# Optimization experiments

Hardware: AMD Instinct MI355X
Metric: run time of the kernel (lower is better)

The kernel has to match this reference:

```python
import jax, jax.numpy as jnp
import numpy as np

B, N, D = 32, 1024, 256

def setup_inputs() -> dict:
    key = jax.random.key(0)
    ks = jax.random.split(key, 7)
    s = 1.0 / np.sqrt(D)
    return {
        "traj": jax.random.normal(ks[0], (B, N, D), dtype=jnp.float32),
        "Wq": jax.random.normal(ks[1], (D, D), dtype=jnp.float32) * s,
        "bq": jax.random.normal(ks[2], (D,), dtype=jnp.float32) * s,
        "Wk": jax.random.normal(ks[3], (D, D), dtype=jnp.float32) * s,
        "bk": jax.random.normal(ks[4], (D,), dtype=jnp.float32) * s,
        "Wv": jax.random.normal(ks[5], (D, D), dtype=jnp.float32) * s,
        "bv": jax.random.normal(ks[6], (D,), dtype=jnp.float32) * s,
    }

def reference(traj, Wq, bq, Wk, bk, Wv, bv):
    # torch nn.Linear: y = x @ W.T + b
    q = jnp.einsum('bnd,ed->bne', traj, Wq) + bq  # [B,N,D]
    k = jnp.einsum('bnd,ed->bne', traj, Wk) + bk  # [B,N,D]
    v = jnp.einsum('bnd,ed->bne', traj, Wv) + bv  # [B,N,D]
    # unscaled dot-product attention (original sums broadcasted Q*K over D)
    scores = jnp.einsum('bnd,bmd->bnm', q, k)     # [B,N,N]
    attn = jax.nn.softmax(scores, axis=-1)        # [B,N,N]
    out = jnp.einsum('bnm,bmd->bnd', attn, v)     # [B,N,D]
    return out
```

## Files before the change

kernel.cpp:

```cpp
#include <hip/hip_runtime.h>

#define NN 1024
#define DD 256

typedef __attribute__((ext_vector_type(8))) _Float16 f16x8;
typedef __attribute__((ext_vector_type(4))) float f32x4;

union H8 { f16x8 v; _Float16 s[8]; };

__device__ __forceinline__ void g2lds16(const void* g, void* l) {
  __builtin_amdgcn_global_load_lds(
      (const __attribute__((address_space(1))) void*)g,
      (__attribute__((address_space(3))) void*)l, 16, 0, 0);
}

__global__ void wconv_kernel(const float* __restrict__ Wq, const float* __restrict__ Wk,
                             const float* __restrict__ Wv, _Float16* __restrict__ pw) {
  int c = blockIdx.x * 256 + threadIdx.x;
  int lane = c & 63;
  int nt = (c >> 6) & 1;
  int kk = (c >> 7) & 7;
  int et = c >> 10;
  int e = et * 32 + nt * 16 + (lane & 15);
  int d = kk * 32 + (lane >> 4) * 8;
  const float* W = (e < 256) ? Wq : (e < 512 ? Wk : Wv);
  const float* src = W + (e & 255) * 256 + d;
  H8 xx;
  for (int j = 0; j < 8; ++j) xx.s[j] = (_Float16)src[j];
  *(f16x8*)(pw + (size_t)c * 8) = xx.v;
}

__global__ __launch_bounds__(256, 2) void proj_kernel(
    const float* __restrict__ traj,
    const float* __restrict__ bq, const float* __restrict__ bk, const float* __restrict__ bv,
    const _Float16* __restrict__ pw,
    _Float16* __restrict__ pq, _Float16* __restrict__ pk, _Float16* __restrict__ pv)
{
  __shared__ alignas(16) _Float16 Wl[2][8192];
  __shared__ alignas(16) _Float16 Cs[4][1280];

  const int t = threadIdx.x;
  const int lane = t & 63, wave = t >> 6;
  const int col16 = lane & 15, quad = lane >> 4;
  const int mt = blockIdx.x >> 1, eh = blockIdx.x & 1;
  const int mbase = mt * 128;
  const int bb = mbase >> 10;

  f16x8 aq[2][8];
  for (int s = 0; s < 2; ++s) {
    const float* ap = traj + (size_t)(mbase + wave * 32 + s * 16 + col16) * DD;
    for (int kk = 0; kk < 8; ++kk) {
      float4 u0 = *(const float4*)(ap + kk * 32 + quad * 8);
      float4 u1 = *(const float4*)(ap + kk * 32 + quad * 8 + 4);
      H8 xx;
      xx.s[0] = (_Float16)u0.x; xx.s[1] = (_Float16)u0.y;
      xx.s[2] = (_Float16)u0.z; xx.s[3] = (_Float16)u0.w;
      xx.s[4] = (_Float16)u1.x; xx.s[5] = (_Float16)u1.y;
      xx.s[6] = (_Float16)u1.z; xx.s[7] = (_Float16)u1.w;
      aq[s][kk] = xx.v;
    }
  }

  const f32x4 zero = {0.f, 0.f, 0.f, 0.f};
  const int et0 = eh * 12;

  for (int i = 0; i < 4; ++i)
    g2lds16(pw + (size_t)et0 * 8192 + (size_t)(i * 256 + t) * 8, Wl[0] + (i * 256 + t) * 8);

  for (int ei = 0; ei < 12; ++ei) {
    __syncthreads();
    if (ei < 11) {
      const _Float16* ws = pw + (size_t)(et0 + ei + 1) * 8192;
      _Float16* wd = Wl[(ei + 1) & 1];
      for (int i = 0; i < 4; ++i)
        g2lds16(ws + (size_t)(i * 256 + t) * 8, wd + (i * 256 + t) * 8);
    }
    const _Float16* wl = Wl[ei & 1];

    f32x4 acc[2][2];
    acc[0][0] = zero; acc[0][1] = zero; acc[1][0] = zero; acc[1][1] = zero;
    for (int kk = 0; kk < 8; ++kk)
      for (int nt = 0; nt < 2; ++nt) {
        f16x8 bw = *(const f16x8*)&wl[((kk * 2 + nt) * 64 + lane) * 8];
        acc[0][nt] = __builtin_amdgcn_mfma_f32_16x16x32_f16(aq[0][kk], bw, acc[0][nt], 0, 0, 0);
        acc[1][nt] = __builtin_amdgcn_mfma_f32_16x16x32_f16(aq[1][kk], bw, acc[1][nt], 0, 0, 0);
      }

    int e0 = eh * 384 + ei * 32;
    int sel = e0 >> 8;
    const float* bias = (sel == 0) ? bq : (sel == 1 ? bk : bv);
    for (int nt = 0; nt < 2; ++nt) {
      float bvl = bias[(e0 & 255) + nt * 16 + col16];
      for (int s = 0; s < 2; ++s) {
        acc[s][nt][0] += bvl; acc[s][nt][1] += bvl;
        acc[s][nt][2] += bvl; acc[s][nt][3] += bvl;
      }
    }

    _Float16* cs = Cs[wave];
    if (sel < 2) {
      for (int s = 0; s < 2; ++s)
        for (int nt = 0; nt < 2; ++nt)
          for (int r = 0; r < 4; ++r)
            cs[(s * 16 + quad * 4 + r) * 40 + nt * 16 + col16] = (_Float16)acc[s][nt][r];
      if (sel == 0) {
        for (int s = 0; s < 2; ++s) {
          f16x8 val = *(const f16x8*)&cs[(s * 16 + col16) * 40 + quad * 8];
          int g = (mbase >> 4) + wave * 2 + s;
          *(f16x8*)(pq + (size_t)((g * 8 + ei) * 64 + lane) * 8) = val;
        }
      } else {
        int kkg = (e0 - 256) >> 5;
        for (int s = 0; s < 2; ++s) {
          f16x8 val = *(const f16x8*)&cs[(s * 16 + col16) * 40 + quad * 8];
          int kgg = ((mbase & 1023) >> 4) + wave * 2 + s;
          *(f16x8*)(pk + (size_t)(((bb * 64 + kgg) * 8 + kkg) * 64 + lane) * 8) = val;
        }
      }
    } else {
      for (int s = 0; s < 2; ++s)
        for (int nt = 0; nt < 2; ++nt)
          for (int r = 0; r < 4; ++r)
            cs[(nt * 16 + col16) * 40 + s * 16 + quad * 4 + r] = (_Float16)acc[s][nt][r];
      int kt32 = ((mbase & 1023) >> 5) + wave;
      for (int dtl = 0; dtl < 2; ++dtl) {
        f16x8 val = *(const f16x8*)&cs[(dtl * 16 + col16) * 40 + quad * 8];
        int dtg = ((e0 - 512) >> 4) + dtl;
        *(f16x8*)(pv + (size_t)(((bb * 32 + kt32) * 16 + dtg) * 64 + lane) * 8) = val;
      }
    }
  }
}

__global__ __launch_bounds__(256, 3) void attn_kernel(
    const _Float16* __restrict__ pq, const _Float16* __restrict__ pk,
    const _Float16* __restrict__ pv, float* __restrict__ out)
{
  __shared__ alignas(16) _Float16 Ks[2][8192];
  __shared__ alignas(16) _Float16 Vs[8192];

  const int t = threadIdx.x;
  const int lane = t & 63, wave = t >> 6;
  const int col16 = lane & 15, quad = lane >> 4;
  const int b = blockIdx.x, qt = blockIdx.y;
  const int qrow0 = b * NN + qt * 64;

  f16x8 aq[8];
  {
    int g = b * 64 + qt * 4 + wave;
    for (int kk = 0; kk < 8; ++kk)
      aq[kk] = *(const f16x8*)(pq + (size_t)((g * 8 + kk) * 64 + lane) * 8);
  }

  float m_i = -3.0e38f, l_i = 0.f;
  f32x4 O[16];
  const f32x4 zero = {0.f, 0.f, 0.f, 0.f};
  for (int dt = 0; dt < 16; ++dt) O[dt] = zero;

  const _Float16* kbb = pk + (size_t)b * 64 * 8 * 64 * 8;
  const _Float16* vbb = pv + (size_t)b * 32 * 16 * 64 * 8;

  for (int i = 0; i < 4; ++i)
    g2lds16(kbb + (size_t)(i * 256 + t) * 8, Ks[0] + (i * 256 + t) * 8);

  for (int kt = 0; kt < 32; ++kt) {
    __syncthreads();
    {
      const _Float16* vg = vbb + (size_t)kt * 8192;
      for (int i = 0; i < 4; ++i)
        g2lds16(vg + (size_t)(i * 256 + t) * 8, Vs + (i * 256 + t) * 8);
      if (kt < 31) {
        const _Float16* kg = kbb + (size_t)(kt + 1) * 8192;
        _Float16* kd = Ks[(kt + 1) & 1];
        for (int i = 0; i < 4; ++i)
          g2lds16(kg + (size_t)(i * 256 + t) * 8, kd + (i * 256 + t) * 8);
      }
    }

    const _Float16* ks = Ks[kt & 1];
    f32x4 S[2]; S[0] = zero; S[1] = zero;
    for (int kk = 0; kk < 8; ++kk)
      for (int nt = 0; nt < 2; ++nt) {
        f16x8 bk_ = *(const f16x8*)&ks[((nt * 8 + kk) * 64 + lane) * 8];
        S[nt] = __builtin_amdgcn_mfma_f32_16x16x32_f16(aq[kk], bk_, S[nt], 0, 0, 0);
      }

    __syncthreads();

    float* Sp = (float*)Ks[kt & 1];
    for (int nt = 0; nt < 2; ++nt)
      for (int r = 0; r < 4; ++r)
        Sp[(wave * 16 + quad * 4 + r) * 36 + nt * 16 + col16] = S[nt][r];
    float sv[8];
    *(f32x4*)&sv[0] = *(const f32x4*)&Sp[(wave * 16 + col16) * 36 + quad * 8];
    *(f32x4*)&sv[4] = *(const f32x4*)&Sp[(wave * 16 + col16) * 36 + quad * 8 + 4];

    float vmax = sv[0];
    for (int j = 1; j < 8; ++j) vmax = fmaxf(vmax, sv[j]);
    vmax = fmaxf(vmax, __shfl_xor(vmax, 16));
    vmax = fmaxf(vmax, __shfl_xor(vmax, 32));
    float nm = fmaxf(m_i, vmax);
    float alpha = __expf(m_i - nm);
    float rs = 0.f;
    H8 px;
    for (int j = 0; j < 8; ++j) {
      float pj = __expf(sv[j] - nm);
      rs += pj;
      px.s[j] = (_Float16)pj;
    }
    rs += __shfl_xor(rs, 16);
    rs += __shfl_xor(rs, 32);
    l_i = l_i * alpha + rs;
    m_i = nm;
    f16x8 ap = px.v;

    if (__ballot(alpha < 1.0f)) {
      float a4[4];
      for (int r = 0; r < 4; ++r) a4[r] = __shfl(alpha, quad * 4 + r);
      for (int dt = 0; dt < 16; ++dt)
        for (int r = 0; r < 4; ++r) O[dt][r] *= a4[r];
    }

    for (int dt = 0; dt < 16; ++dt) {
      f16x8 bv_ = *(const f16x8*)&Vs[(dt * 64 + lane) * 8];
      O[dt] = __builtin_amdgcn_mfma_f32_16x16x32_f16(ap, bv_, O[dt], 0, 0, 0);
    }
  }

  float linv[4];
  for (int r = 0; r < 4; ++r) linv[r] = 1.0f / __shfl(l_i, quad * 4 + r);
  for (int r = 0; r < 4; ++r) {
    float* orow = out + (size_t)(qrow0 + wave * 16 + quad * 4 + r) * DD;
    for (int dt = 0; dt < 16; ++dt)
      orow[dt * 16 + col16] = O[dt][r] * linv[r];
  }
}

extern "C" void kernel_launch(void* const* d_in, const int* in_sizes, int n_in,
                              void* d_out, int out_size, void* d_ws, size_t ws_size,
                              hipStream_t stream) {
  const float* traj = (const float*)d_in[0];
  const float* Wq   = (const float*)d_in[1];
  const float* bq   = (const float*)d_in[2];
  const float* Wk   = (const float*)d_in[3];
  const float* bk   = (const float*)d_in[4];
  const float* Wv   = (const float*)d_in[5];
  const float* bv   = (const float*)d_in[6];

  _Float16* pq = (_Float16*)d_ws;
  _Float16* pk = pq + (size_t)32768 * 256;
  _Float16* pv = pk + (size_t)32768 * 256;
  _Float16* pw = pv + (size_t)32768 * 256;

  wconv_kernel<<<96, 256, 0, stream>>>(Wq, Wk, Wv, pw);
  proj_kernel<<<512, 256, 0, stream>>>(traj, bq, bk, bv, pw, pq, pk, pv);
  attn_kernel<<<dim3(32, 16), 256, 0, stream>>>(pq, pk, pv, (float*)d_out);
}
```

Measured before the change: 170.3 us.

## Double query rows per attention block, double-buffer V, prepack traj, restructure projection

The attention kernel now processes 128 query rows per block (two 16-row tiles per wave), so each K/V tile loaded into LDS is reused twice as much. V gets double-buffered alongside K, and scores go through a dedicated per-wave LDS scratch, which removes one block barrier per iteration. A separate kernel prepacks traj into fp16 MFMA layout. The projection kernel is split four ways over output columns and loads its whole weight slice into LDS up front. The cost is half as many attention blocks (256 on a large GPU), more registers per wave, an extra pass over traj, and a larger grid for the projection.

```diff
diff --git a/kernel.cpp b/kernel.cpp
--- a/kernel.cpp
+++ b/kernel.cpp
@@ -12,6 +12,17 @@
   __builtin_amdgcn_global_load_lds(
       (const __attribute__((address_space(1))) void*)g,
       (__attribute__((address_space(3))) void*)l, 16, 0, 0);
+}
+
+__global__ void apack_kernel(const float* __restrict__ traj, _Float16* __restrict__ pa) {
+  int c = blockIdx.x * 256 + threadIdx.x;
+  int lane = c & 63;
+  int kk = (c >> 6) & 7;
+  int g = c >> 9;
+  const float* src = traj + (size_t)(g * 16 + (lane & 15)) * 256 + kk * 32 + (lane >> 4) * 8;
+  H8 xx;
+  for (int j = 0; j < 8; ++j) xx.s[j] = (_Float16)src[j];
+  *(f16x8*)(pa + (size_t)c * 8) = xx.v;
 }
 
 __global__ void wconv_kernel(const float* __restrict__ Wq, const float* __restrict__ Wk,
@@ -30,63 +41,49 @@
   *(f16x8*)(pw + (size_t)c * 8) = xx.v;
 }
 
-__global__ __launch_bounds__(256, 2) void proj_kernel(
-    const float* __restrict__ traj,
+__global__ __launch_bounds__(256, 1) void proj_kernel(
+    const _Float16* __restrict__ pa,
     const float* __restrict__ bq, const float* __restrict__ bk, const float* __restrict__ bv,
     const _Float16* __restrict__ pw,
     _Float16* __restrict__ pq, _Float16* __restrict__ pk, _Float16* __restrict__ pv)
 {
-  __shared__ alignas(16) _Float16 Wl[2][8192];
+  __shared__ alignas(16) _Float16 Wl[49152];
   __shared__ alignas(16) _Float16 Cs[4][1280];
 
   const int t = threadIdx.x;
   const int lane = t & 63, wave = t >> 6;
   const int col16 = lane & 15, quad = lane >> 4;
-  const int mt = blockIdx.x >> 1, eh = blockIdx.x & 1;
+  const int mt = blockIdx.x >> 2, eq = blockIdx.x & 3;
   const int mbase = mt * 128;
   const int bb = mbase >> 10;
 
+  {
+    const _Float16* ws = pw + (size_t)eq * 6 * 8192;
+    for (int i = 0; i < 24; ++i)
+      g2lds16(ws + (size_t)(i * 256 + t) * 8, Wl + (i * 256 + t) * 8);
+  }
+
   f16x8 aq[2][8];
   for (int s = 0; s < 2; ++s) {
-    const float* ap = traj + (size_t)(mbase + wave * 32 + s * 16 + col16) * DD;
-    for (int kk = 0; kk < 8; ++kk) {
-      float4 u0 = *(const float4*)(ap + kk * 32 + quad * 8);
-      float4 u1 = *(const float4*)(ap + kk * 32 + quad * 8 + 4);
-      H8 xx;
-      xx.s[0] = (_Float16)u0.x; xx.s[1] = (_Float16)u0.y;
-      xx.s[2] = (_Float16)u0.z; xx.s[3] = (_Float16)u0.w;
-      xx.s[4] = (_Float16)u1.x; xx.s[5] = (_Float16)u1.y;
-      xx.s[6] = (_Float16)u1.z; xx.s[7] = (_Float16)u1.w;
-      aq[s][kk] = xx.v;
-    }
-  }
-
+    int g = (mbase >> 4) + wave * 2 + s;
+    for (int kk = 0; kk < 8; ++kk)
+      aq[s][kk] = *(const f16x8*)(pa + (size_t)((g * 8 + kk) * 64 + lane) * 8);
+  }
+
+  __syncthreads();
   const f32x4 zero = {0.f, 0.f, 0.f, 0.f};
-  const int et0 = eh * 12;
-
-  for (int i = 0; i < 4; ++i)
-    g2lds16(pw + (size_t)et0 * 8192 + (size_t)(i * 256 + t) * 8, Wl[0] + (i * 256 + t) * 8);
-
-  for (int ei = 0; ei < 12; ++ei) {
-    __syncthreads();
-    if (ei < 11) {
-      const _Float16* ws = pw + (size_t)(et0 + ei + 1) * 8192;
-      _Float16* wd = Wl[(ei + 1) & 1];
-      for (int i = 0; i < 4; ++i)
-        g2lds16(ws + (size_t)(i * 256 + t) * 8, wd + (i * 256 + t) * 8);
-    }
-    const _Float16* wl = Wl[ei & 1];
-
+
+  for (int ei = 0; ei < 6; ++ei) {
     f32x4 acc[2][2];
     acc[0][0] = zero; acc[0][1] = zero; acc[1][0] = zero; acc[1][1] = zero;
     for (int kk = 0; kk < 8; ++kk)
       for (int nt = 0; nt < 2; ++nt) {
-        f16x8 bw = *(const f16x8*)&wl[((kk * 2 + nt) * 64 + lane) * 8];
+        f16x8 bw = *(const f16x8*)&Wl[((ei * 16 + kk * 2 + nt) * 64 + lane) * 8];
         acc[0][nt] = __builtin_amdgcn_mfma_f32_16x16x32_f16(aq[0][kk], bw, acc[0][nt], 0, 0, 0);
         acc[1][nt] = __builtin_amdgcn_mfma_f32_16x16x32_f16(aq[1][kk], bw, acc[1][nt], 0, 0, 0);
       }
 
-    int e0 = eh * 384 + ei * 32;
+    int e0 = eq * 192 + ei * 32;
     int sel = e0 >> 8;
     const float* bias = (sel == 0) ? bq : (sel == 1 ? bk : bv);
     for (int nt = 0; nt < 2; ++nt) {
@@ -104,10 +101,11 @@
           for (int r = 0; r < 4; ++r)
             cs[(s * 16 + quad * 4 + r) * 40 + nt * 16 + col16] = (_Float16)acc[s][nt][r];
       if (sel == 0) {
+        int kkq = e0 >> 5;
         for (int s = 0; s < 2; ++s) {
           f16x8 val = *(const f16x8*)&cs[(s * 16 + col16) * 40 + quad * 8];
           int g = (mbase >> 4) + wave * 2 + s;
-          *(f16x8*)(pq + (size_t)((g * 8 + ei) * 64 + lane) * 8) = val;
+          *(f16x8*)(pq + (size_t)((g * 8 + kkq) * 64 + lane) * 8) = val;
         }
       } else {
         int kkg = (e0 - 256) >> 5;
@@ -132,107 +130,123 @@
   }
 }
 
-__global__ __launch_bounds__(256, 3) void attn_kernel(
+__global__ __launch_bounds__(256, 1) void attn_kernel(
     const _Float16* __restrict__ pq, const _Float16* __restrict__ pk,
     const _Float16* __restrict__ pv, float* __restrict__ out)
 {
   __shared__ alignas(16) _Float16 Ks[2][8192];
-  __shared__ alignas(16) _Float16 Vs[8192];
+  __shared__ alignas(16) _Float16 Vs[2][8192];
+  __shared__ alignas(16) float Sp[4][1056];
 
   const int t = threadIdx.x;
   const int lane = t & 63, wave = t >> 6;
   const int col16 = lane & 15, quad = lane >> 4;
   const int b = blockIdx.x, qt = blockIdx.y;
-  const int qrow0 = b * NN + qt * 64;
-
-  f16x8 aq[8];
-  {
-    int g = b * 64 + qt * 4 + wave;
+  const int qrow0 = b * NN + qt * 128;
+
+  f16x8 aq[2][8];
+  for (int s = 0; s < 2; ++s) {
+    int g = b * 64 + qt * 8 + wave * 2 + s;
     for (int kk = 0; kk < 8; ++kk)
-      aq[kk] = *(const f16x8*)(pq + (size_t)((g * 8 + kk) * 64 + lane) * 8);
-  }
-
-  float m_i = -3.0e38f, l_i = 0.f;
-  f32x4 O[16];
+      aq[s][kk] = *(const f16x8*)(pq + (size_t)((g * 8 + kk) * 64 + lane) * 8);
+  }
+
+  float m_i[2] = {-3.0e38f, -3.0e38f}, l_i[2] = {0.f, 0.f};
+  f32x4 O[2][16];
   const f32x4 zero = {0.f, 0.f, 0.f, 0.f};
-  for (int dt = 0; dt < 16; ++dt) O[dt] = zero;
+  for (int s = 0; s < 2; ++s)
+    for (int dt = 0; dt < 16; ++dt) O[s][dt] = zero;
 
   const _Float16* kbb = pk + (size_t)b * 64 * 8 * 64 * 8;
   const _Float16* vbb = pv + (size_t)b * 32 * 16 * 64 * 8;
 
   for (int i = 0; i < 4; ++i)
     g2lds16(kbb + (size_t)(i * 256 + t) * 8, Ks[0] + (i * 256 + t) * 8);
+  for (int i = 0; i < 4; ++i)
+    g2lds16(vbb + (size_t)(i * 256 + t) * 8, Vs[0] + (i * 256 + t) * 8);
 
   for (int kt = 0; kt < 32; ++kt) {
     __syncthreads();
-    {
-      const _Float16* vg = vbb + (size_t)kt * 8192;
+    if (kt < 31) {
+      const _Float16* kg = kbb + (size_t)(kt + 1) * 8192;
+      const _Float16* vg = vbb + (size_t)(kt + 1) * 8192;
+      _Float16* kd = Ks[(kt + 1) & 1];
+      _Float16* vd = Vs[(kt + 1) & 1];
       for (int i = 0; i < 4; ++i)
-        g2lds16(vg + (size_t)(i * 256 + t) * 8, Vs + (i * 256 + t) * 8);
-      if (kt < 31) {
-        const _Float16* kg = kbb + (size_t)(kt + 1) * 8192;
-        _Float16* kd = Ks[(kt + 1) & 1];
-        for (int i = 0; i < 4; ++i)
-          g2lds16(kg + (size_t)(i * 256 + t) * 8, kd + (i * 256 + t) * 8);
-      }
+        g2lds16(kg + (size_t)(i * 256 + t) * 8, kd + (i * 256 + t) * 8);
+      for (int i = 0; i < 4; ++i)
+        g2lds16(vg + (size_t)(i * 256 + t) * 8, vd + (i * 256 + t) * 8);
     }
 
     const _Float16* ks = Ks[kt & 1];
-    f32x4 S[2]; S[0] = zero; S[1] = zero;
-    for (int kk = 0; kk < 8; ++kk)
-      for (int nt = 0; nt < 2; ++nt) {
-        f16x8 bk_ = *(const f16x8*)&ks[((nt * 8 + kk) * 64 + lane) * 8];
-        S[nt] = __builtin_amdgcn_mfma_f32_16x16x32_f16(aq[kk], bk_, S[nt], 0, 0, 0);
-      }
-
-    __syncthreads();
-
-    float* Sp = (float*)Ks[kt & 1];
-    for (int nt = 0; nt < 2; ++nt)
-      for (int r = 0; r < 4; ++r)
-        Sp[(wave * 16 + quad * 4 + r) * 36 + nt * 16 + col16] = S[nt][r];
-    float sv[8];
-    *(f32x4*)&sv[0] = *(const f32x4*)&Sp[(wave * 16 + col16) * 36 + quad * 8];
-    *(f32x4*)&sv[4] = *(const f32x4*)&Sp[(wave * 16 + col16) * 36 + quad * 8 + 4];
-
-    float vmax = sv[0];
-    for (int j = 1; j < 8; ++j) vmax = fmaxf(vmax, sv[j]);
-    vmax = fmaxf(vmax, __shfl_xor(vmax, 16));
-    vmax = fmaxf(vmax, __shfl_xor(vmax, 32));
-    float nm = fmaxf(m_i, vmax);
-    float alpha = __expf(m_i - nm);
-    float rs = 0.f;
-    H8 px;
-    for (int j = 0; j < 8; ++j) {
-      float pj = __expf(sv[j] - nm);
-      rs += pj;
-      px.s[j] = (_Float16)pj;
-    }
-    rs += __shfl_xor(rs, 16);
-    rs += __shfl_xor(rs, 32);
-    l_i = l_i * alpha + rs;
-    m_i = nm;
-    f16x8 ap = px.v;
-
-    if (__ballot(alpha < 1.0f)) {
-      float a4[4];
-      for (int r = 0; r < 4; ++r) a4[r] = __shfl(alpha, quad * 4 + r);
+    f32x4 S[2][2];
+    S[0][0] = zero; S[0][1] = zero; S[1][0] = zero; S[1][1] = zero;
+    for (int kk = 0; kk < 8; ++kk) {
+      f16x8 bk0 = *(const f16x8*)&ks[((0 * 8 + kk) * 64 + lane) * 8];
+      f16x8 bk1 = *(const f16x8*)&ks[((1 * 8 + kk) * 64 + lane) * 8];
+      S[0][0] = __builtin_amdgcn_mfma_f32_16x16x32_f16(aq[0][kk], bk0, S[0][0], 0, 0, 0);
+      S[0][1] = __builtin_amdgcn_mfma_f32_16x16x32_f16(aq[0][kk], bk1, S[0][1], 0, 0, 0);
+      S[1][0] = __builtin_amdgcn_mfma_f32_16x16x32_f16(aq[1][kk], bk0, S[1][0], 0, 0, 0);
+      S[1][1] = __builtin_amdgcn_mfma_f32_16x16x32_f16(aq[1][kk], bk1, S[1][1], 0, 0, 0);
+    }
+
+    float* sp = Sp[wave];
+    for (int s = 0; s < 2; ++s)
+      for (int nt = 0; nt < 2; ++nt)
+        for (int r = 0; r < 4; ++r)
+          sp[(s * 16 + quad * 4 + r) * 33 + nt * 16 + col16] = S[s][nt][r];
+
+    f16x8 ap[2];
+    float alpha[2];
+    for (int s = 0; s < 2; ++s) {
+      float sv[8];
+      *(f32x4*)&sv[0] = *(const f32x4*)&sp[(s * 16 + col16) * 33 + quad * 8];
+      *(f32x4*)&sv[4] = *(const f32x4*)&sp[(s * 16 + col16) * 33 + quad * 8 + 4];
+      float vmax = sv[0];
+      for (int j = 1; j < 8; ++j) vmax = fmaxf(vmax, sv[j]);
+      vmax = fmaxf(vmax, __shfl_xor(vmax, 16));
+      vmax = fmaxf(vmax, __shfl_xor(vmax, 32));
+      float nm = fmaxf(m_i[s], vmax);
+      alpha[s] = __expf(m_i[s] - nm);
+      float rs = 0.f;
+      H8 px;
+      for (int j = 0; j < 8; ++j) {
+        float pj = __expf(sv[j] - nm);
+        rs += pj;
+        px.s[j] = (_Float16)pj;
+      }
+      rs += __shfl_xor(rs, 16);
+      rs += __shfl_xor(rs, 32);
+      l_i[s] = l_i[s] * alpha[s] + rs;
+      m_i[s] = nm;
+      ap[s] = px.v;
+    }
+
+    if (__ballot(fminf(alpha[0], alpha[1]) < 1.0f)) {
+      for (int s = 0; s < 2; ++s) {
+        float a4[4];
+        for (int r = 0; r < 4; ++r) a4[r] = __shfl(alpha[s], quad * 4 + r);
+        for (int dt = 0; dt < 16; ++dt)
+          for (int r = 0; r < 4; ++r) O[s][dt][r] *= a4[r];
+      }
+    }
+
+    const _Float16* vs = Vs[kt & 1];
+    for (int dt = 0; dt < 16; ++dt) {
+      f16x8 bv_ = *(const f16x8*)&vs[(dt * 64 + lane) * 8];
+      O[0][dt] = __builtin_amdgcn_mfma_f32_16x16x32_f16(ap[0], bv_, O[0][dt], 0, 0, 0);
+      O[1][dt] = __builtin_amdgcn_mfma_f32_16x16x32_f16(ap[1], bv_, O[1][dt], 0, 0, 0);
+    }
+  }
+
+  for (int s = 0; s < 2; ++s) {
+    float linv[4];
+    for (int r = 0; r < 4; ++r) linv[r] = 1.0f / __shfl(l_i[s], quad * 4 + r);
+    for (int r = 0; r < 4; ++r) {
+      float* orow = out + (size_t)(qrow0 + wave * 32 + s * 16 + quad * 4 + r) * DD;
       for (int dt = 0; dt < 16; ++dt)
-        for (int r = 0; r < 4; ++r) O[dt][r] *= a4[r];
-    }
-
-    for (int dt = 0; dt < 16; ++dt) {
-      f16x8 bv_ = *(const f16x8*)&Vs[(dt * 64 + lane) * 8];
-      O[dt] = __builtin_amdgcn_mfma_f32_16x16x32_f16(ap, bv_, O[dt], 0, 0, 0);
-    }
-  }
-
-  float linv[4];
-  for (int r = 0; r < 4; ++r) linv[r] = 1.0f / __shfl(l_i, quad * 4 + r);
-  for (int r = 0; r < 4; ++r) {
-    float* orow = out + (size_t)(qrow0 + wave * 16 + quad * 4 + r) * DD;
-    for (int dt = 0; dt < 16; ++dt)
-      orow[dt * 16 + col16] = O[dt][r] * linv[r];
+        orow[dt * 16 + col16] = O[s][dt][r] * linv[r];
+    }
   }
 }
 
@@ -250,9 +264,11 @@
   _Float16* pq = (_Float16*)d_ws;
   _Float16* pk = pq + (size_t)32768 * 256;
   _Float16* pv = pk + (size_t)32768 * 256;
-  _Float16* pw = pv + (size_t)32768 * 256;
-
+  _Float16* pa = pv + (size_t)32768 * 256;
+  _Float16* pw = pa + (size_t)32768 * 256;
+
+  apack_kernel<<<4096, 256, 0, stream>>>(traj, pa);
   wconv_kernel<<<96, 256, 0, stream>>>(Wq, Wk, Wv, pw);
-  proj_kernel<<<512, 256, 0, stream>>>(traj, bq, bk, bv, pw, pq, pk, pv);
-  attn_kernel<<<dim3(32, 16), 256, 0, stream>>>(pq, pk, pv, (float*)d_out);
-}
+  proj_kernel<<<1024, 256, 0, stream>>>(pa, bq, bk, bv, pw, pq, pk, pv);
+  attn_kernel<<<dim3(32, 8), 256, 0, stream>>>(pq, pk, pv, (float*)d_out);
+}
```

New measurement: 220.9 us. 1.3x slower.
